# Optimization experiments

Measured on AMD Instinct MI355X. Metric: run time of the kernel, lower is better.

Reference implementation:

```python
import jax, jax.numpy as jnp
import numpy as np

B, S, D, H = 4, 2048, 1024, 16
HD = D // H  # head dim = 64

def setup_inputs() -> dict:
    key = jax.random.key(0)
    ks = jax.random.split(key, 6)
    scale = 0.02
    x = jax.random.normal(ks[0], (B, S, D), dtype=jnp.float32)
    Wq = jax.random.normal(ks[1], (D, D), dtype=jnp.float32) * scale
    Wk = jax.random.normal(ks[2], (D, D), dtype=jnp.float32) * scale
    Wv = jax.random.normal(ks[3], (D, D), dtype=jnp.float32) * scale
    Wo = jax.random.normal(ks[4], (D, D), dtype=jnp.float32) * scale
    bo = jnp.zeros((D,), dtype=jnp.float32)
    return {"x": x, "Wq": Wq, "Wk": Wk, "Wv": Wv, "Wo": Wo, "bo": bo}

def reference(x, Wq, Wk, Wv, Wo, bo):
    b, s, d = x.shape
    h, hd = H, HD
    # project and split heads -> [b, h, s, hd]
    def split_heads(t):
        return t.reshape(b, s, h, hd).transpose(0, 2, 1, 3)
    q = split_heads(x @ Wq)
    k = split_heads(x @ Wk)
    v = split_heads(x @ Wv)
    # causal attention with full score matrix (faithful to the naive impl)
    scores = jnp.einsum('bhqd,bhkd->bhqk', q, k)
    causal = jnp.triu(jnp.ones((s, s), dtype=bool), k=1)  # True above diagonal
    scores = jnp.where(causal, -jnp.inf, scores)
    attn = jax.nn.softmax(scores / jnp.sqrt(jnp.float32(hd)), axis=-1)
    ctx = jnp.einsum('bhqk,bhkd->bhqd', attn, v)
    ctx = ctx.transpose(0, 2, 1, 3).reshape(b, s, d)
    return ctx @ Wo + bo
```

## Files before the change

### kernel.cpp

```cpp
#include <hip/hip_runtime.h>
#include <math.h>
#include <stdint.h>

typedef __bf16 bf16;
typedef bf16 bf16x2 __attribute__((ext_vector_type(2)));
typedef bf16 bf16x8 __attribute__((ext_vector_type(8)));
typedef float floatx4 __attribute__((ext_vector_type(4)));

static constexpr int Sq = 2048, Dm = 1024, Hh = 16, HDim = 64;

#define GAS __attribute__((address_space(1)))
#define LAS __attribute__((address_space(3)))

__device__ __forceinline__ void dma16(const void* g, void* l) {
    __builtin_amdgcn_global_load_lds((const GAS void*)g, (LAS void*)l, 16, 0, 0);
}

__device__ __forceinline__ uint32_t pk_bf16(float a, float b) {
    bf16x2 t;
    t[0] = (bf16)a;
    t[1] = (bf16)b;
    return __builtin_bit_cast(uint32_t, t);
}

__global__ __launch_bounds__(256)
void prep_all(const float* __restrict__ Wq, const float* __restrict__ Wk,
              const float* __restrict__ Wv, const float* __restrict__ Wo,
              bf16* __restrict__ Wt,
              const float* __restrict__ x, bf16* __restrict__ xb)
{
    const int t = threadIdx.x;
    if (blockIdx.z == 4) {
        const int b = blockIdx.y * 16 + blockIdx.x;
        const size_t base = ((size_t)b * 256 + t) * 8;
#pragma unroll
        for (int it = 0; it < 16; it++) {
            const size_t i = base + (size_t)it * 524288;
            float4 f0 = *(const float4*)(x + i);
            float4 f1 = *(const float4*)(x + i + 4);
            bf16x8 v;
            v[0]=(bf16)f0.x; v[1]=(bf16)f0.y; v[2]=(bf16)f0.z; v[3]=(bf16)f0.w;
            v[4]=(bf16)f1.x; v[5]=(bf16)f1.y; v[6]=(bf16)f1.z; v[7]=(bf16)f1.w;
            *(bf16x8*)(xb + i) = v;
        }
        return;
    }
    const int w = blockIdx.z;
    const float* W = (w == 0) ? Wq : (w == 1) ? Wk : (w == 2) ? Wv : Wo;
    bf16* dst = Wt + (size_t)w * 1024 * 1024;
    const int k0 = blockIdx.x * 64, n0 = blockIdx.y * 64;
    __shared__ uint32_t Tl[64][33];
    {
        const int c8 = (t & 7) * 8;
        const int kp = t >> 3;
        const float* r0 = W + (size_t)(k0 + 2 * kp) * 1024 + n0 + c8;
        const float* r1 = r0 + 1024;
        float4 a0 = *(const float4*)r0, a1 = *(const float4*)(r0 + 4);
        float4 b0 = *(const float4*)r1, b1 = *(const float4*)(r1 + 4);
        float ra[8] = {a0.x, a0.y, a0.z, a0.w, a1.x, a1.y, a1.z, a1.w};
        float rb[8] = {b0.x, b0.y, b0.z, b0.w, b1.x, b1.y, b1.z, b1.w};
#pragma unroll
        for (int j = 0; j < 8; j++)
            Tl[c8 + j][kp] = pk_bf16(ra[j], rb[j]);
    }
    __syncthreads();
    {
        const int c = t >> 2, dq = (t & 3) * 8;
        uint32_t d[8];
#pragma unroll
        for (int i = 0; i < 8; i++) d[i] = Tl[c][dq + i];
        uint32_t* o = (uint32_t*)(dst + (size_t)(n0 + c) * 1024 + k0 + dq * 2);
        *(uint4*)o       = make_uint4(d[0], d[1], d[2], d[3]);
        *(uint4*)(o + 4) = make_uint4(d[4], d[5], d[6], d[7]);
    }
}

template <int AMODE>
__global__ __launch_bounds__(256, 2)
void qkv_gemm(const float* __restrict__ x, const bf16* __restrict__ xb,
              const bf16* __restrict__ Wt,
              bf16* __restrict__ Qb, bf16* __restrict__ Kb, bf16* __restrict__ VT)
{
    const int zz = blockIdx.z;
    const bf16* Wsel = Wt + (size_t)zz * 1024 * 1024;

    __shared__ __align__(16) unsigned char smem[34816];
    bf16 (*As1)[64] = (bf16(*)[64])smem;
    bf16 (*As0)[72] = (bf16(*)[72])smem;
    bf16 (*Bs)[64]  = (bf16(*)[64])(smem + (AMODE ? 16384 : 18432));

    const int tid  = threadIdx.x;
    const int wave = tid >> 6, lane = tid & 63, quad = lane >> 4, l16 = lane & 15;
    const int bm = blockIdx.x * 128, bn = blockIdx.y * 128;
    const int wm = (wave >> 1) * 64, wn = (wave & 1) * 64;

    floatx4 acc[4][4];
#pragma unroll
    for (int i = 0; i < 4; i++)
#pragma unroll
        for (int j = 0; j < 4; j++) acc[i][j] = (floatx4){0.f, 0.f, 0.f, 0.f};

    for (int k0 = 0; k0 < 1024; k0 += 64) {
        __syncthreads();
#pragma unroll
        for (int i = 0; i < 4; i++) {
            const int row = wave * 32 + i * 8 + (lane >> 3);
            const int lb  = (lane & 7) ^ (row & 7);
            const bf16* g = Wsel + (size_t)(bn + row) * 1024 + k0 + lb * 8;
            dma16((const void*)g, (void*)&Bs[wave * 32 + i * 8][0]);
        }
        if (AMODE) {
#pragma unroll
            for (int i = 0; i < 4; i++) {
                const int row = wave * 32 + i * 8 + (lane >> 3);
                const int lb  = (lane & 7) ^ (row & 7);
                const bf16* g = xb + (size_t)(bm + row) * 1024 + k0 + lb * 8;
                dma16((const void*)g, (void*)&As1[wave * 32 + i * 8][0]);
            }
        } else {
#pragma unroll
            for (int it = 0; it < 2; it++) {
                const int r  = (tid >> 2) + it * 64;
                const int cq = (tid & 3) * 16;
                const float* src = x + (size_t)(bm + r) * 1024 + k0 + cq;
                float4 f0 = *(const float4*)src,       f1 = *(const float4*)(src + 4);
                float4 f2 = *(const float4*)(src + 8), f3 = *(const float4*)(src + 12);
                bf16x8 v0, v1;
                v0[0]=(bf16)f0.x; v0[1]=(bf16)f0.y; v0[2]=(bf16)f0.z; v0[3]=(bf16)f0.w;
                v0[4]=(bf16)f1.x; v0[5]=(bf16)f1.y; v0[6]=(bf16)f1.z; v0[7]=(bf16)f1.w;
                v1[0]=(bf16)f2.x; v1[1]=(bf16)f2.y; v1[2]=(bf16)f2.z; v1[3]=(bf16)f2.w;
                v1[4]=(bf16)f3.x; v1[5]=(bf16)f3.y; v1[6]=(bf16)f3.z; v1[7]=(bf16)f3.w;
                *(bf16x8*)&As0[r][cq]     = v0;
                *(bf16x8*)&As0[r][cq + 8] = v1;
            }
        }
        __syncthreads();

#pragma unroll
        for (int kk = 0; kk < 2; kk++) {
            bf16x8 a[4], b[4];
#pragma unroll
            for (int tm = 0; tm < 4; tm++) {
                const int m = wm + tm * 16 + l16;
                if (AMODE) {
                    const int phys = (kk * 4 + quad) ^ (m & 7);
                    a[tm] = *(const bf16x8*)&As1[m][phys * 8];
                } else {
                    a[tm] = *(const bf16x8*)&As0[m][kk * 32 + quad * 8];
                }
            }
#pragma unroll
            for (int tn = 0; tn < 4; tn++) {
                const int n = wn + tn * 16 + l16;
                const int phys = (kk * 4 + quad) ^ (n & 7);
                b[tn] = *(const bf16x8*)&Bs[n][phys * 8];
            }
#pragma unroll
            for (int tm = 0; tm < 4; tm++)
#pragma unroll
                for (int tn = 0; tn < 4; tn++)
                    acc[tm][tn] = __builtin_amdgcn_mfma_f32_16x16x32_bf16(a[tm], b[tn], acc[tm][tn], 0, 0, 0);
        }
    }

    if (zz < 2) {
        bf16* dst = (zz == 0) ? Qb : Kb;
        const float sc = (zz == 1) ? 0.18033688f : 1.0f;
#pragma unroll
        for (int tm = 0; tm < 4; tm++)
#pragma unroll
            for (int tn = 0; tn < 4; tn++)
#pragma unroll
                for (int r = 0; r < 4; r++) {
                    const int m = bm + wm + tm * 16 + quad * 4 + r;
                    const int n = bn + wn + tn * 16 + l16;
                    const int bb = m >> 11, s = m & 2047;
                    const int h = n >> 6, d = n & 63;
                    dst[(((size_t)(bb * Hh + h)) * Sq + s) * HDim + d] = (bf16)(acc[tm][tn][r] * sc);
                }
    } else {
        __syncthreads();
        bf16 (*CT)[136] = (bf16(*)[136])smem;
#pragma unroll
        for (int tm = 0; tm < 4; tm++)
#pragma unroll
            for (int tn = 0; tn < 4; tn++)
#pragma unroll
                for (int r = 0; r < 4; r++) {
                    const int ml = wm + tm * 16 + quad * 4 + r;
                    const int nl = wn + tn * 16 + l16;
                    CT[nl][ml] = (bf16)acc[tm][tn][r];
                }
        __syncthreads();
        const int nl = tid >> 1, part = tid & 1;
        const int n = bn + nl, h = n >> 6, d = n & 63;
        const int bbv = bm >> 11, s0v = bm & 2047;
        bf16* o = VT + (((size_t)(bbv * Hh + h)) * HDim + d) * Sq + s0v + part * 64;
#pragma unroll
        for (int i = 0; i < 8; i++)
            *(bf16x8*)(o + i * 8) = *(const bf16x8*)&CT[nl][part * 64 + i * 8];
    }
}

__global__ __launch_bounds__(128)
void attn(const bf16* __restrict__ Qb, const bf16* __restrict__ Kb,
          const bf16* __restrict__ VTg, bf16* __restrict__ Cx)
{
    const int bh = blockIdx.x;
    const int bl = bh >> 4, h = bh & 15;

    __shared__ __align__(16) bf16 Kl[64][64];
    __shared__ __align__(16) bf16 Vt[64][64];
    __shared__ __align__(16) bf16 PlT[2][32][72];

    const int tid  = threadIdx.x;
    const int wave = tid >> 6, lane = tid & 63, quad = lane >> 4, l16 = lane & 15;

    const int srow = wave * 32 + (lane >> 3);
    const int lb   = (lane & 7) ^ (lane >> 3);

    for (int pass = 0; pass < 2; pass++) {
        const int qt = (pass == 0) ? (int)blockIdx.y : 31 - (int)blockIdx.y;
        const int q0 = qt * 64 + wave * 32;
        const int nk = qt + 1;

        bf16x8 bq[2][2];
#pragma unroll
        for (int nt = 0; nt < 2; nt++) {
            const bf16* Qrow = Qb + ((size_t)bh * Sq + q0 + nt * 16 + l16) * HDim;
            bq[nt][0] = *(const bf16x8*)(Qrow + quad * 8);
            bq[nt][1] = *(const bf16x8*)(Qrow + 32 + quad * 8);
        }

        floatx4 acc[4][2];
#pragma unroll
        for (int i = 0; i < 4; i++)
#pragma unroll
            for (int j = 0; j < 2; j++) acc[i][j] = (floatx4){0.f, 0.f, 0.f, 0.f};
        float l_part[2] = {0.f, 0.f};

        const bf16* kp = Kb  + ((size_t)bh * Sq + srow) * HDim + lb * 8;
        const bf16* vp = VTg + ((size_t)bh * HDim + srow) * Sq + lb * 8;

        auto tile = [&](bool masked) {
            __syncthreads();
#pragma unroll
            for (int i = 0; i < 4; i++) {
                dma16((const void*)(kp + (size_t)(i * 8) * HDim), (void*)&Kl[wave * 32 + i * 8][0]);
                dma16((const void*)(vp + (size_t)(i * 8) * Sq),  (void*)&Vt[wave * 32 + i * 8][0]);
            }
            __syncthreads();

            floatx4 sT[4][2];
#pragma unroll
            for (int mt = 0; mt < 4; mt++) {
                const int kr = mt * 16 + l16;
                bf16x8 ak0 = *(const bf16x8*)&Kl[kr][(quad ^ (kr & 7)) * 8];
                bf16x8 ak1 = *(const bf16x8*)&Kl[kr][((4 + quad) ^ (kr & 7)) * 8];
#pragma unroll
                for (int nt = 0; nt < 2; nt++) {
                    floatx4 z = (floatx4){0.f, 0.f, 0.f, 0.f};
                    z = __builtin_amdgcn_mfma_f32_16x16x32_bf16(ak0, bq[nt][0], z, 0, 0, 0);
                    z = __builtin_amdgcn_mfma_f32_16x16x32_bf16(ak1, bq[nt][1], z, 0, 0, 0);
                    sT[mt][nt] = z;
                }
            }

            if (masked) {
#pragma unroll
                for (int mt = 0; mt < 4; mt++)
#pragma unroll
                    for (int nt = 0; nt < 2; nt++)
#pragma unroll
                        for (int r = 0; r < 4; r++) {
                            const int keyl  = mt * 16 + quad * 4 + r;
                            const int qrowl = wave * 32 + nt * 16 + l16;
                            if (keyl > qrowl) sT[mt][nt][r] = -1e30f;
                        }
            }

#pragma unroll
            for (int nt = 0; nt < 2; nt++) {
                float rs = 0.f;
#pragma unroll
                for (int mt = 0; mt < 4; mt++)
#pragma unroll
                    for (int r = 0; r < 4; r++) {
                        const float e = __builtin_amdgcn_exp2f(sT[mt][nt][r]);
                        sT[mt][nt][r] = e;
                        rs += e;
                    }
                l_part[nt] += rs;
            }

#pragma unroll
            for (int mt = 0; mt < 4; mt++)
#pragma unroll
                for (int nt = 0; nt < 2; nt++) {
                    uint2 pk;
                    pk.x = pk_bf16(sT[mt][nt][0], sT[mt][nt][1]);
                    pk.y = pk_bf16(sT[mt][nt][2], sT[mt][nt][3]);
                    *(uint2*)&PlT[wave][nt * 16 + l16][mt * 16 + quad * 4] = pk;
                }

#pragma unroll
            for (int ks = 0; ks < 2; ks++) {
                bf16x8 bp[2];
#pragma unroll
                for (int nt = 0; nt < 2; nt++)
                    bp[nt] = *(const bf16x8*)&PlT[wave][nt * 16 + l16][ks * 32 + quad * 8];
#pragma unroll
                for (int mt = 0; mt < 4; mt++) {
                    const int vr = mt * 16 + l16;
                    bf16x8 av = *(const bf16x8*)&Vt[vr][((ks * 4 + quad) ^ (vr & 7)) * 8];
#pragma unroll
                    for (int nt = 0; nt < 2; nt++)
                        acc[mt][nt] = __builtin_amdgcn_mfma_f32_16x16x32_bf16(av, bp[nt], acc[mt][nt], 0, 0, 0);
                }
            }
        };

        for (int kt = 0; kt < nk - 1; kt++) {
            tile(false);
            kp += 64 * HDim;
            vp += 64;
        }
        tile(true);

#pragma unroll
        for (int nt = 0; nt < 2; nt++) {
            float rs = l_part[nt];
            rs += __shfl_xor(rs, 16, 64);
            rs += __shfl_xor(rs, 32, 64);
            const float inv = __builtin_amdgcn_rcpf(rs);
            const int qrow = q0 + nt * 16 + l16;
#pragma unroll
            for (int mt = 0; mt < 4; mt++) {
                uint2 pk;
                pk.x = pk_bf16(acc[mt][nt][0] * inv, acc[mt][nt][1] * inv);
                pk.y = pk_bf16(acc[mt][nt][2] * inv, acc[mt][nt][3] * inv);
                *(uint2*)(Cx + ((size_t)(bl * Sq + qrow)) * Dm + h * HDim + mt * 16 + quad * 4) = pk;
            }
        }
    }
}

__global__ __launch_bounds__(256, 2)
void out_gemm(const bf16* __restrict__ Cx, const bf16* __restrict__ WtO,
              const float* __restrict__ bo, float* __restrict__ out, int mbase)
{
    __shared__ __align__(16) bf16 As2[128][64];
    __shared__ __align__(16) bf16 Bs2[128][64];

    const int tid  = threadIdx.x;
    const int wave = tid >> 6, lane = tid & 63, quad = lane >> 4, l16 = lane & 15;
    const int bm = blockIdx.x * 128, bn = blockIdx.y * 128;
    const int wm = (wave >> 1) * 64, wn = (wave & 1) * 64;

    floatx4 acc[4][4];
#pragma unroll
    for (int i = 0; i < 4; i++)
#pragma unroll
        for (int j = 0; j < 4; j++) acc[i][j] = (floatx4){0.f, 0.f, 0.f, 0.f};

    for (int k0 = 0; k0 < 1024; k0 += 64) {
        __syncthreads();
#pragma unroll
        for (int i = 0; i < 4; i++) {
            const int row = wave * 32 + i * 8 + (lane >> 3);
            const int lb  = (lane & 7) ^ (row & 7);
            const bf16* ga = Cx  + (size_t)(bm + row) * 1024 + k0 + lb * 8;
            const bf16* gb = WtO + (size_t)(bn + row) * 1024 + k0 + lb * 8;
            dma16((const void*)ga, (void*)&As2[wave * 32 + i * 8][0]);
            dma16((const void*)gb, (void*)&Bs2[wave * 32 + i * 8][0]);
        }
        __syncthreads();

#pragma unroll
        for (int kk = 0; kk < 2; kk++) {
            bf16x8 a[4], b[4];
#pragma unroll
            for (int tm = 0; tm < 4; tm++) {
                const int m = wm + tm * 16 + l16;
                const int phys = (kk * 4 + quad) ^ (m & 7);
                a[tm] = *(const bf16x8*)&As2[m][phys * 8];
            }
#pragma unroll
            for (int tn = 0; tn < 4; tn++) {
                const int n = wn + tn * 16 + l16;
                const int phys = (kk * 4 + quad) ^ (n & 7);
                b[tn] = *(const bf16x8*)&Bs2[n][phys * 8];
            }
#pragma unroll
            for (int tm = 0; tm < 4; tm++)
#pragma unroll
                for (int tn = 0; tn < 4; tn++)
                    acc[tm][tn] = __builtin_amdgcn_mfma_f32_16x16x32_bf16(a[tm], b[tn], acc[tm][tn], 0, 0, 0);
        }
    }

#pragma unroll
    for (int tm = 0; tm < 4; tm++)
#pragma unroll
        for (int tn = 0; tn < 4; tn++)
#pragma unroll
            for (int r = 0; r < 4; r++) {
                const int m = bm + wm + tm * 16 + quad * 4 + r;
                const int n = bn + wn + tn * 16 + l16;
                out[(size_t)(mbase + m) * 1024 + n] = acc[tm][tn][r] + bo[n];
            }
}

extern "C" void kernel_launch(void* const* d_in, const int* in_sizes, int n_in,
                              void* d_out, int out_size, void* d_ws, size_t ws_size,
                              hipStream_t stream)
{
    const float* x  = (const float*)d_in[0];
    const float* Wq = (const float*)d_in[1];
    const float* Wk = (const float*)d_in[2];
    const float* Wv = (const float*)d_in[3];
    const float* Wo = (const float*)d_in[4];
    const float* bo = (const float*)d_in[5];
    float* out = (float*)d_out;

    const size_t M1 = 1024 * 1024;
    const size_t XE = (size_t)8192 * 1024;

    if (ws_size >= (size_t)72 * 1024 * 1024) {
        bf16* Wt = (bf16*)d_ws;
        bf16* xb = Wt + 4 * M1;
        bf16* Qb = xb + XE;
        bf16* Kb = Qb + XE;
        bf16* VT = Kb + XE;
        bf16* Cx = xb;

        prep_all<<<dim3(16, 16, 5), 256, 0, stream>>>(Wq, Wk, Wv, Wo, Wt, x, xb);
        qkv_gemm<1><<<dim3(64, 8, 3), 256, 0, stream>>>(x, xb, Wt, Qb, Kb, VT);
        attn<<<dim3(64, 16), 128, 0, stream>>>(Qb, Kb, VT, Cx);
        out_gemm<<<dim3(64, 8), 256, 0, stream>>>(Cx, Wt + 3 * M1, bo, out, 0);
    } else {
        bf16* Wt = (bf16*)d_ws;
        bf16* Qb = Wt + 4 * M1;
        bf16* Kb = Qb + XE;
        bf16* VT = Kb + XE;
        bf16* Cx = VT + XE;

        prep_all<<<dim3(16, 16, 4), 256, 0, stream>>>(Wq, Wk, Wv, Wo, Wt, nullptr, nullptr);
        qkv_gemm<0><<<dim3(64, 8, 3), 256, 0, stream>>>(x, nullptr, Wt, Qb, Kb, VT);
        const size_t chunk = (size_t)2 * Hh * Sq * HDim;
        for (int c = 0; c < 2; c++) {
            attn<<<dim3(32, 16), 128, 0, stream>>>(Qb + c * chunk, Kb + c * chunk,
                                                   VT + c * chunk, Cx);
            out_gemm<<<dim3(32, 8), 256, 0, stream>>>(Cx, Wt + 3 * M1, bo, out, c * 4096);
        }
    }
}
```

Measured before the change: 239.9 us.

## Double-buffer K/V tiles in attention with async prefetch and wave priority

The attention kernel now keeps two LDS buffers for K and V. It issues the DMA for the next tile before computing on the current one, and uses vmcnt waits with raw barriers instead of two __syncthreads per tile, so global loads overlap with MFMA work. It also replaces the padded P transpose buffer with an XOR-swizzled unpadded layout, and raises wave priority around the MFMA sections. The cost is double the K/V LDS footprint, and correctness now relies on the hand-counted vmcnt values and the barrier placement.

New measurement: 240.7 us. About the same (+0.3%).

```diff
diff --git a/kernel.cpp b/kernel.cpp
--- a/kernel.cpp
+++ b/kernel.cpp
@@ -209,9 +209,9 @@
     const int bh = blockIdx.x;
     const int bl = bh >> 4, h = bh & 15;
 
-    __shared__ __align__(16) bf16 Kl[64][64];
-    __shared__ __align__(16) bf16 Vt[64][64];
-    __shared__ __align__(16) bf16 PlT[2][32][72];
+    __shared__ __align__(16) bf16 Kl[2][64][64];
+    __shared__ __align__(16) bf16 Vt[2][64][64];
+    __shared__ __align__(16) bf16 PlT[2][32][64];
 
     const int tid  = threadIdx.x;
     const int wave = tid >> 6, lane = tid & 63, quad = lane >> 4, l16 = lane & 15;
@@ -242,21 +242,27 @@
         const bf16* kp = Kb  + ((size_t)bh * Sq + srow) * HDim + lb * 8;
         const bf16* vp = VTg + ((size_t)bh * HDim + srow) * Sq + lb * 8;
 
-        auto tile = [&](bool masked) {
-            __syncthreads();
+        auto stage = [&](int nb) {
 #pragma unroll
             for (int i = 0; i < 4; i++) {
-                dma16((const void*)(kp + (size_t)(i * 8) * HDim), (void*)&Kl[wave * 32 + i * 8][0]);
-                dma16((const void*)(vp + (size_t)(i * 8) * Sq),  (void*)&Vt[wave * 32 + i * 8][0]);
-            }
-            __syncthreads();
+                dma16((const void*)(kp + (size_t)(i * 8) * HDim), (void*)&Kl[nb][wave * 32 + i * 8][0]);
+                dma16((const void*)(vp + (size_t)(i * 8) * Sq),  (void*)&Vt[nb][wave * 32 + i * 8][0]);
+            }
+            kp += 64 * HDim;
+            vp += 64;
+        };
+
+        auto tile = [&](int nb, bool masked) {
+            const bf16 (*Ksm)[64] = Kl[nb];
+            const bf16 (*Vsm)[64] = Vt[nb];
 
             floatx4 sT[4][2];
+            __builtin_amdgcn_s_setprio(1);
 #pragma unroll
             for (int mt = 0; mt < 4; mt++) {
                 const int kr = mt * 16 + l16;
-                bf16x8 ak0 = *(const bf16x8*)&Kl[kr][(quad ^ (kr & 7)) * 8];
-                bf16x8 ak1 = *(const bf16x8*)&Kl[kr][((4 + quad) ^ (kr & 7)) * 8];
+                bf16x8 ak0 = *(const bf16x8*)&Ksm[kr][(quad ^ (kr & 7)) * 8];
+                bf16x8 ak1 = *(const bf16x8*)&Ksm[kr][((4 + quad) ^ (kr & 7)) * 8];
 #pragma unroll
                 for (int nt = 0; nt < 2; nt++) {
                     floatx4 z = (floatx4){0.f, 0.f, 0.f, 0.f};
@@ -265,6 +271,7 @@
                     sT[mt][nt] = z;
                 }
             }
+            __builtin_amdgcn_s_setprio(0);
 
             if (masked) {
 #pragma unroll
@@ -300,32 +307,46 @@
                     uint2 pk;
                     pk.x = pk_bf16(sT[mt][nt][0], sT[mt][nt][1]);
                     pk.y = pk_bf16(sT[mt][nt][2], sT[mt][nt][3]);
-                    *(uint2*)&PlT[wave][nt * 16 + l16][mt * 16 + quad * 4] = pk;
+                    const int row  = nt * 16 + l16;
+                    const int boff = (mt * 32 + quad * 8) ^ ((row & 7) << 4);
+                    *(uint2*)((char*)&PlT[wave][row][0] + boff) = pk;
                 }
 
 #pragma unroll
             for (int ks = 0; ks < 2; ks++) {
                 bf16x8 bp[2];
 #pragma unroll
-                for (int nt = 0; nt < 2; nt++)
-                    bp[nt] = *(const bf16x8*)&PlT[wave][nt * 16 + l16][ks * 32 + quad * 8];
+                for (int nt = 0; nt < 2; nt++) {
+                    const int row  = nt * 16 + l16;
+                    const int boff = (ks * 64 + quad * 16) ^ ((row & 7) << 4);
+                    bp[nt] = *(const bf16x8*)((const char*)&PlT[wave][row][0] + boff);
+                }
+                __builtin_amdgcn_s_setprio(1);
 #pragma unroll
                 for (int mt = 0; mt < 4; mt++) {
                     const int vr = mt * 16 + l16;
-                    bf16x8 av = *(const bf16x8*)&Vt[vr][((ks * 4 + quad) ^ (vr & 7)) * 8];
+                    bf16x8 av = *(const bf16x8*)&Vsm[vr][((ks * 4 + quad) ^ (vr & 7)) * 8];
 #pragma unroll
                     for (int nt = 0; nt < 2; nt++)
                         acc[mt][nt] = __builtin_amdgcn_mfma_f32_16x16x32_bf16(av, bp[nt], acc[mt][nt], 0, 0, 0);
                 }
+                __builtin_amdgcn_s_setprio(0);
             }
         };
 
+        stage(0);
         for (int kt = 0; kt < nk - 1; kt++) {
-            tile(false);
-            kp += 64 * HDim;
-            vp += 64;
-        }
-        tile(true);
+            const int cur = kt & 1;
+            stage(cur ^ 1);
+            asm volatile("s_waitcnt vmcnt(8)" ::: "memory");
+            __builtin_amdgcn_s_barrier();
+            tile(cur, false);
+            __builtin_amdgcn_s_barrier();
+        }
+        asm volatile("s_waitcnt vmcnt(0)" ::: "memory");
+        __builtin_amdgcn_s_barrier();
+        tile((nk - 1) & 1, true);
+        __builtin_amdgcn_s_barrier();
 
 #pragma unroll
         for (int nt = 0; nt < 2; nt++) {
```
